# Kernel optimization log

Measured on AMD Instinct MI355X. Metric: run time of the kernel, lower is better.

The kernel has to match this reference:

```python
import jax, jax.numpy as jnp
import numpy as np

B, S, D, H, NL, FE = 2, 1024, 1024, 16, 6, 4
HD = D // H
DFF = D * FE
EPS = 1e-5


def setup_inputs() -> dict:
    key = jax.random.key(0)
    ks = jax.random.split(key, 12)
    sd = 0.02
    n = lambda k, sh: (jax.random.normal(k, sh, jnp.float32) * sd)
    return {
        "x": jax.random.normal(ks[0], (B, S, D), jnp.float32),
        "pos": n(ks[1], (1, S, D)),
        "Wq": n(ks[2], (NL, HD, HD)), "bq": jnp.zeros((NL, HD), jnp.float32),
        "Wk": n(ks[3], (NL, HD, HD)), "bk": jnp.zeros((NL, HD), jnp.float32),
        "Wv": n(ks[4], (NL, HD, HD)), "bv": jnp.zeros((NL, HD), jnp.float32),
        "Wfc": n(ks[5], (NL, D, D)), "bfc": jnp.zeros((NL, D), jnp.float32),
        "ln1_w": jnp.ones((NL, D), jnp.float32), "ln1_b": jnp.zeros((NL, D), jnp.float32),
        "ln2_w": jnp.ones((NL, D), jnp.float32), "ln2_b": jnp.zeros((NL, D), jnp.float32),
        "W1": n(ks[6], (NL, D, DFF)), "b1": jnp.zeros((NL, DFF), jnp.float32),
        "W2": n(ks[7], (NL, DFF, D)), "b2": jnp.zeros((NL, D), jnp.float32),
        "lnf_w": jnp.ones((D,), jnp.float32), "lnf_b": jnp.zeros((D,), jnp.float32),
    }


def _ln(z, w, b):
    m = jnp.mean(z, axis=-1, keepdims=True)
    v = jnp.mean(jnp.square(z - m), axis=-1, keepdims=True)
    return (z - m) * jax.lax.rsqrt(v + EPS) * w + b


def reference(x, pos, Wq, bq, Wk, bk, Wv, bv, Wfc, bfc,
              ln1_w, ln1_b, ln2_w, ln2_b, W1, b1, W2, b2, lnf_w, lnf_b):
    Bx, Sx, Dx = x.shape
    causal = jnp.tril(jnp.ones((Sx, Sx), bool))  # [S,S], broadcast over b,h
    y = x + pos[:, :Sx, :]
    scale = 1.0 / jnp.sqrt(jnp.float32(HD))
    for i in range(NL):
        yh = y.reshape(Bx, Sx, H, HD)
        # per-head Linear with weights SHARED across heads (as in source)
        q = yh @ Wq[i] + bq[i]
        k = yh @ Wk[i] + bk[i]
        v = yh @ Wv[i] + bv[i]
        score = jnp.einsum("bqhd,bkhd->bhqk", q, k)
        # masked_fill(-1e20) BEFORE scaling, as in source
        score = jnp.where(causal, score, jnp.float32(-1e20)) * scale
        attn = jax.nn.softmax(score, axis=-1)
        o = jnp.einsum("bhqk,bkhd->bqhd", attn, v).reshape(Bx, Sx, D)
        o = o @ Wfc[i] + bfc[i]
        add = _ln(o + y, ln1_w[i], ln1_b[i])
        ff = jax.nn.gelu(add @ W1[i] + b1[i], approximate=False) @ W2[i] + b2[i]
        y = _ln(ff + add, ln2_w[i], ln2_b[i])
    return _ln(y, lnf_w, lnf_b)
```

## Files before the change

kernel.cpp:

```cpp
#include <hip/hip_runtime.h>
#include <hip/hip_bf16.h>
#include <math.h>

#define B_   2
#define S_   1024
#define D_   1024
#define H_   16
#define HD_  64
#define NL_  6
#define DFF_ 4096

typedef __bf16 bf16_t;
typedef bf16_t bf16x8 __attribute__((ext_vector_type(8)));
typedef bf16_t bf16x4 __attribute__((ext_vector_type(4)));
typedef float  f32x4  __attribute__((ext_vector_type(4)));

__device__ __forceinline__ float gelu_exact(float x) {
    return 0.5f * x * (1.0f + erff(x * 0.70710678118654752f));
}

__device__ __forceinline__ void gload16(const bf16_t* g, bf16_t* l) {
    __builtin_amdgcn_global_load_lds(
        (const __attribute__((address_space(1))) void*)g,
        (__attribute__((address_space(3))) void*)l, 16, 0, 0);
}

__global__ __launch_bounds__(256) void add_pos_kernel(
    const float* __restrict__ x, const float* __restrict__ pos,
    float* __restrict__ y, bf16_t* __restrict__ yb)
{
    int idx = blockIdx.x * 256 + threadIdx.x;
    f32x4 xv = *(const f32x4*)&x[idx * 4];
    f32x4 pv = *(const f32x4*)&pos[(idx & 262143) * 4];
    f32x4 o = xv + pv;
    *(f32x4*)&y[idx * 4] = o;
    *(bf16x4*)&yb[idx * 4] = __builtin_convertvector(o, bf16x4);
}

__global__ __launch_bounds__(256) void qkv_mfma_kernel(
    const bf16_t* __restrict__ yb,
    const float* __restrict__ Wq, const float* __restrict__ bq,
    const float* __restrict__ Wk, const float* __restrict__ bk,
    const float* __restrict__ Wv, const float* __restrict__ bv,
    bf16_t* __restrict__ q, bf16_t* __restrict__ k, bf16_t* __restrict__ v)
{
    __shared__ __align__(16) bf16_t As[128][72];
    __shared__ __align__(16) bf16_t Wt[3][64][72];

    int tid = threadIdx.x;
    long m0 = (long)blockIdx.x * 128;

#pragma unroll
    for (int it = 0; it < 4; ++it) {
        int c = it * 256 + tid;
        int row = c >> 3, col = (c & 7) * 8;
        *(bf16x8*)&As[row][col] = *(const bf16x8*)&yb[(m0 + row) * 64 + col];
    }
#pragma unroll
    for (int it = 0; it < 16; ++it) {
        int i = it * 256 + tid;
        int r = i >> 6, c = i & 63;
        Wt[0][c][r] = (bf16_t)Wq[i];
        Wt[1][c][r] = (bf16_t)Wk[i];
        Wt[2][c][r] = (bf16_t)Wv[i];
    }
    __syncthreads();

    int wave = tid >> 6, lane = tid & 63;
    int quad = lane >> 4, l16 = lane & 15;
    int wm = wave * 32;

    bf16x8 a[2][2];
#pragma unroll
    for (int i = 0; i < 2; ++i)
#pragma unroll
        for (int ks = 0; ks < 2; ++ks)
            a[i][ks] = *(bf16x8*)&As[wm + i * 16 + l16][ks * 32 + quad * 8];

    f32x4 acc[3][2][4];
#pragma unroll
    for (int o = 0; o < 3; ++o)
#pragma unroll
        for (int i = 0; i < 2; ++i)
#pragma unroll
            for (int j = 0; j < 4; ++j) acc[o][i][j] = (f32x4)0.f;

#pragma unroll
    for (int o = 0; o < 3; ++o)
#pragma unroll
        for (int j = 0; j < 4; ++j) {
            bf16x8 b0 = *(bf16x8*)&Wt[o][j * 16 + l16][quad * 8];
            bf16x8 b1 = *(bf16x8*)&Wt[o][j * 16 + l16][32 + quad * 8];
#pragma unroll
            for (int i = 0; i < 2; ++i) {
                acc[o][i][j] = __builtin_amdgcn_mfma_f32_16x16x32_bf16(a[i][0], b0, acc[o][i][j], 0, 0, 0);
                acc[o][i][j] = __builtin_amdgcn_mfma_f32_16x16x32_bf16(a[i][1], b1, acc[o][i][j], 0, 0, 0);
            }
        }

    bf16_t* outs[3] = { q, k, v };
    const float* biases[3] = { bq, bk, bv };
#pragma unroll
    for (int o = 0; o < 3; ++o)
#pragma unroll
        for (int j = 0; j < 4; ++j) {
            int col = j * 16 + l16;
            float bias = biases[o][col];
#pragma unroll
            for (int i = 0; i < 2; ++i) {
                long rbase = m0 + wm + i * 16 + quad * 4;
#pragma unroll
                for (int r = 0; r < 4; ++r)
                    outs[o][(rbase + r) * 64 + col] = (bf16_t)(acc[o][i][j][r] + bias);
            }
        }
}

__global__ __launch_bounds__(256) void vtrans_kernel(
    const bf16_t* __restrict__ vb, bf16_t* __restrict__ vT)
{
    __shared__ __align__(16) bf16_t L[32][72];
    int tid = threadIdx.x;
    int s0 = blockIdx.x * 32;
    int bh = blockIdx.y;
    int b = bh >> 4, h = bh & 15;
    int sr = tid >> 3, dc = (tid & 7) * 8;
    *(bf16x8*)&L[sr][dc] =
        *(const bf16x8*)&vb[(((long)b * S_ + s0 + sr) * H_ + h) * HD_ + dc];
    __syncthreads();
    int dr = tid >> 2, sg = (tid & 3) * 8;
    bf16x8 o;
#pragma unroll
    for (int j = 0; j < 8; ++j) o[j] = L[sg + j][dr];
    *(bf16x8*)&vT[((long)bh * HD_ + dr) * S_ + s0 + sg] = o;
}

__global__ __launch_bounds__(256) void attn_mfma_kernel(
    const bf16_t* __restrict__ Q, const bf16_t* __restrict__ K,
    const bf16_t* __restrict__ VT, bf16_t* __restrict__ Ob)
{
    __shared__ __align__(16) bf16_t Ks[32][72];
    __shared__ __align__(16) bf16_t Vt[64][40];
    __shared__ __align__(16) bf16_t Ps[4][16][40];

    int tid = threadIdx.x;
    int wave = tid >> 6, lane = tid & 63;
    int quad = lane >> 4, l16 = lane & 15;
    int q0 = blockIdx.x * 64;
    int bh = blockIdx.y;
    int b = bh >> 4, h = bh & 15;
    int qw = q0 + wave * 16;
    const float scale = 0.125f;
    const float MASKED = -1.25e19f;

    const bf16_t* Qbase = Q + (((long)b * S_ + qw + l16) * H_ + h) * HD_;
    bf16x8 aq0 = *(const bf16x8*)&Qbase[quad * 8];
    bf16x8 aq1 = *(const bf16x8*)&Qbase[32 + quad * 8];

    float mrun = -3.0e38f, lrun = 0.f;
    f32x4 oacc[4];
#pragma unroll
    for (int n = 0; n < 4; ++n) oacc[n] = (f32x4)0.f;

    int srow = tid >> 3, scol = (tid & 7) * 8;
    int vdr = tid >> 2, vkg = (tid & 3) * 8;
    const bf16_t* VTbase = VT + ((long)bh * HD_ + vdr) * S_ + vkg;
    int qg = qw + l16;

    int nkt = (q0 + 64) / 32;
    for (int kt = 0; kt < nkt; ++kt) {
        int k0 = kt * 32;
        __syncthreads();
        *(bf16x8*)&Ks[srow][scol] =
            *(const bf16x8*)&K[(((long)b * S_ + k0 + srow) * H_ + h) * HD_ + scol];
        *(bf16x8*)&Vt[vdr][vkg] = *(const bf16x8*)&VTbase[k0];
        __syncthreads();

        if (k0 > qw + 15) continue;

        f32x4 sc[2];
        sc[0] = (f32x4)0.f; sc[1] = (f32x4)0.f;
#pragma unroll
        for (int n = 0; n < 2; ++n) {
            bf16x8 ak0 = *(bf16x8*)&Ks[n * 16 + l16][quad * 8];
            bf16x8 ak1 = *(bf16x8*)&Ks[n * 16 + l16][32 + quad * 8];
            sc[n] = __builtin_amdgcn_mfma_f32_16x16x32_bf16(ak0, aq0, sc[n], 0, 0, 0);
            sc[n] = __builtin_amdgcn_mfma_f32_16x16x32_bf16(ak1, aq1, sc[n], 0, 0, 0);
        }
        float pmax = MASKED;
#pragma unroll
        for (int n = 0; n < 2; ++n)
#pragma unroll
            for (int r = 0; r < 4; ++r) {
                int kv = k0 + n * 16 + quad * 4 + r;
                float sv = (kv <= qg) ? sc[n][r] * scale : MASKED;
                sc[n][r] = sv;
                pmax = fmaxf(pmax, sv);
            }
        pmax = fmaxf(pmax, __shfl_xor(pmax, 16));
        pmax = fmaxf(pmax, __shfl_xor(pmax, 32));
        float mnew = fmaxf(mrun, pmax);
        float ls = 0.f;
#pragma unroll
        for (int n = 0; n < 2; ++n)
#pragma unroll
            for (int r = 0; r < 4; ++r) {
                float pv = __expf(sc[n][r] - mnew);
                sc[n][r] = pv;
                ls += pv;
            }
        ls += __shfl_xor(ls, 16);
        ls += __shfl_xor(ls, 32);
        float alpha = __expf(mrun - mnew);
        lrun = lrun * alpha + ls;
        mrun = mnew;

        *(bf16x4*)&Ps[wave][l16][quad * 4]      = __builtin_convertvector(sc[0], bf16x4);
        *(bf16x4*)&Ps[wave][l16][16 + quad * 4] = __builtin_convertvector(sc[1], bf16x4);

        f32x4 av;
#pragma unroll
        for (int r = 0; r < 4; ++r) av[r] = __shfl(alpha, quad * 4 + r);

        bf16x8 pa = *(bf16x8*)&Ps[wave][l16][quad * 8];
#pragma unroll
        for (int n = 0; n < 4; ++n) {
            bf16x8 bv = *(bf16x8*)&Vt[n * 16 + l16][quad * 8];
            oacc[n] = __builtin_amdgcn_mfma_f32_16x16x32_bf16(pa, bv, oacc[n] * av, 0, 0, 0);
        }
    }

    float inv = 1.0f / lrun;
    f32x4 iv;
#pragma unroll
    for (int r = 0; r < 4; ++r) iv[r] = __shfl(inv, quad * 4 + r);
#pragma unroll
    for (int r = 0; r < 4; ++r) {
        long rowbase = (((long)b * S_ + qw + quad * 4 + r) * H_ + h) * HD_;
#pragma unroll
        for (int n = 0; n < 4; ++n)
            Ob[rowbase + n * 16 + l16] = (bf16_t)(oacc[n][r] * iv[r]);
    }
}

__global__ void tconv_kernel(const float* __restrict__ W, bf16_t* __restrict__ Wt,
                             int Kd, int Nd)
{
    __shared__ float t[32][33];
    int tx = threadIdx.x, ty = threadIdx.y;
    int bx = blockIdx.x, by = blockIdx.y;
#pragma unroll
    for (int i = 0; i < 4; ++i)
        t[ty + i * 8][tx] = W[(size_t)(by * 32 + ty + i * 8) * Nd + bx * 32 + tx];
    __syncthreads();
#pragma unroll
    for (int i = 0; i < 4; ++i)
        Wt[(size_t)(bx * 32 + ty + i * 8) * Kd + by * 32 + tx] = (bf16_t)t[tx][ty + i * 8];
}

__global__ __launch_bounds__(256) void gemm_bt_kernel(
    const bf16_t* __restrict__ A, const bf16_t* __restrict__ Bt,
    const float* __restrict__ bias, float* __restrict__ Cf,
    bf16_t* __restrict__ Cb, int M, int N, int K, int act, size_t pstride)
{
    __shared__ __align__(16) bf16_t As[3][128 * 32];
    __shared__ __align__(16) bf16_t Bs[3][64 * 32];
    int tid = threadIdx.x;
    int wave = tid >> 6, lane = tid & 63;
    int quad = lane >> 4, l16 = lane & 15;
    int m0 = blockIdx.x * 128;
    int n0 = blockIdx.y * 64;
    int Kc = K / gridDim.z;
    int kbeg = blockIdx.z * Kc;
    float* Cfp = Cf ? Cf + (size_t)blockIdx.z * pstride : nullptr;

    int wm = (wave >> 1) * 64, wn = (wave & 1) * 32;

    int srow = lane >> 2;
    int sslot = (lane & 3) ^ (srow & 3);
    int rslot = (quad ^ (l16 & 3)) * 8;

    f32x4 acc[4][2];
#pragma unroll
    for (int i = 0; i < 4; ++i)
#pragma unroll
        for (int j = 0; j < 2; ++j) acc[i][j] = (f32x4)0.f;

    const bf16_t* Ab = A + (size_t)(m0 + srow) * K + sslot * 8;
    const bf16_t* Bb = Bt + (size_t)(n0 + wave * 16 + srow) * K + sslot * 8;
    int seg0 = wave * 2;
    int nt = Kc >> 5;

    #define STAGE(t, buf) do {                                                      \
        int kk_ = kbeg + (t) * 32;                                                  \
        gload16(Ab + (size_t)seg0 * 16 * K + kk_, &As[(buf)][seg0 * 512]);          \
        gload16(Ab + (size_t)(seg0 + 1) * 16 * K + kk_, &As[(buf)][(seg0+1) * 512]);\
        gload16(Bb + kk_, &Bs[(buf)][wave * 512]);                                  \
    } while (0)

    #define COMPUTE(buf) do {                                                       \
        bf16x8 af[4], bfr[2];                                                       \
        _Pragma("unroll")                                                           \
        for (int i = 0; i < 4; ++i)                                                 \
            af[i] = *(bf16x8*)&As[(buf)][(wm + i * 16 + l16) * 32 + rslot];         \
        _Pragma("unroll")                                                           \
        for (int j = 0; j < 2; ++j)                                                 \
            bfr[j] = *(bf16x8*)&Bs[(buf)][(wn + j * 16 + l16) * 32 + rslot];        \
        _Pragma("unroll")                                                           \
        for (int i = 0; i < 4; ++i)                                                 \
            _Pragma("unroll")                                                       \
            for (int j = 0; j < 2; ++j)                                             \
                acc[i][j] = __builtin_amdgcn_mfma_f32_16x16x32_bf16(                \
                    af[i], bfr[j], acc[i][j], 0, 0, 0);                             \
    } while (0)

    STAGE(0, 0);
    STAGE(1, 1);

    int cur = 0, pf = 2;
    for (int t = 0; t < nt - 1; ++t) {
        asm volatile("s_waitcnt vmcnt(3)" ::: "memory");
        __builtin_amdgcn_s_barrier();
        __builtin_amdgcn_sched_barrier(0);
        if (t + 2 < nt) STAGE(t + 2, pf);
        COMPUTE(cur);
        cur = (cur == 2) ? 0 : cur + 1;
        pf  = (pf  == 2) ? 0 : pf  + 1;
    }
    asm volatile("s_waitcnt vmcnt(0)" ::: "memory");
    __builtin_amdgcn_s_barrier();
    __builtin_amdgcn_sched_barrier(0);
    COMPUTE(cur);

    #undef STAGE
    #undef COMPUTE

#pragma unroll
    for (int j = 0; j < 2; ++j) {
        int col = n0 + wn + j * 16 + l16;
        float bv = (bias && blockIdx.z == 0) ? bias[col] : 0.f;
#pragma unroll
        for (int i = 0; i < 4; ++i) {
            int rbase = m0 + wm + i * 16 + quad * 4;
#pragma unroll
            for (int r = 0; r < 4; ++r) {
                float vv = acc[i][j][r] + bv;
                if (act == 1) vv = gelu_exact(vv);
                if (Cfp) Cfp[(size_t)(rbase + r) * N + col] = vv;
                if (Cb) Cb[(size_t)(rbase + r) * N + col] = (bf16_t)vv;
            }
        }
    }
}

__global__ __launch_bounds__(256) void ln_fused_kernel(
    const float* __restrict__ a0, const float* __restrict__ a1,
    const float* __restrict__ b,
    const float* __restrict__ w, const float* __restrict__ beta,
    float* __restrict__ out, bf16_t* __restrict__ outb)
{
    long row = blockIdx.x;
    int tid = threadIdx.x;
    f32x4 z = *(const f32x4*)&a0[row * D_ + tid * 4];
    if (a1) z += *(const f32x4*)&a1[row * D_ + tid * 4];
    if (b)  z += *(const f32x4*)&b[row * D_ + tid * 4];
    float s  = z[0] + z[1] + z[2] + z[3];
    float ss = z[0]*z[0] + z[1]*z[1] + z[2]*z[2] + z[3]*z[3];
#pragma unroll
    for (int off = 32; off >= 1; off >>= 1) {
        s  += __shfl_down(s, off);
        ss += __shfl_down(ss, off);
    }
    __shared__ float red[8];
    int lane = tid & 63, wid = tid >> 6;
    if (lane == 0) { red[wid * 2] = s; red[wid * 2 + 1] = ss; }
    __syncthreads();
    s  = red[0] + red[2] + red[4] + red[6];
    ss = red[1] + red[3] + red[5] + red[7];
    float mean = s * (1.0f / D_);
    float var  = ss * (1.0f / D_) - mean * mean;
    float rs = rsqrtf(var + 1e-5f);
    f32x4 wv = *(const f32x4*)&w[tid * 4];
    f32x4 bv = *(const f32x4*)&beta[tid * 4];
    f32x4 o = (z - mean) * rs * wv + bv;
    *(f32x4*)&out[row * D_ + tid * 4] = o;
    if (outb) *(bf16x4*)&outb[row * D_ + tid * 4] = __builtin_convertvector(o, bf16x4);
}

extern "C" void kernel_launch(void* const* d_in, const int* in_sizes, int n_in,
                              void* d_out, int out_size, void* d_ws, size_t ws_size,
                              hipStream_t stream)
{
    (void)in_sizes; (void)n_in; (void)out_size; (void)ws_size;
    const float* x    = (const float*)d_in[0];
    const float* pos  = (const float*)d_in[1];
    const float* Wq   = (const float*)d_in[2];
    const float* bq   = (const float*)d_in[3];
    const float* Wk   = (const float*)d_in[4];
    const float* bk   = (const float*)d_in[5];
    const float* Wv   = (const float*)d_in[6];
    const float* bv   = (const float*)d_in[7];
    const float* Wfc  = (const float*)d_in[8];
    const float* bfc  = (const float*)d_in[9];
    const float* ln1w = (const float*)d_in[10];
    const float* ln1b = (const float*)d_in[11];
    const float* ln2w = (const float*)d_in[12];
    const float* ln2b = (const float*)d_in[13];
    const float* W1   = (const float*)d_in[14];
    const float* b1   = (const float*)d_in[15];
    const float* W2   = (const float*)d_in[16];
    const float* b2   = (const float*)d_in[17];
    const float* lnfw = (const float*)d_in[18];
    const float* lnfb = (const float*)d_in[19];

    const size_t MB = 1 << 20;
    char* ws = (char*)d_ws;
    float*  y    = (float*)(ws);
    bf16_t* yb   = (bf16_t*)(ws + 8 * MB);
    bf16_t* qb   = (bf16_t*)(ws + 12 * MB);
    bf16_t* kb   = (bf16_t*)(ws + 16 * MB);
    bf16_t* vb   = (bf16_t*)(ws + 20 * MB);
    bf16_t* ob   = (bf16_t*)(ws + 24 * MB);
    float*  t1a  = (float*)(ws + 12 * MB);
    float*  t1b  = (float*)(ws + 28 * MB);
    float*  t2a  = (float*)(ws + 12 * MB);
    float*  t2b  = (float*)(ws + 20 * MB);
    float*  add  = (float*)(ws + 28 * MB);
    bf16_t* addb = (bf16_t*)(ws + 36 * MB);
    bf16_t* vTb  = (bf16_t*)(ws + 40 * MB);
    bf16_t* ffb  = (bf16_t*)(ws + 40 * MB);
    bf16_t* WT   = (bf16_t*)(ws + 56 * MB);

    const size_t pstride_wfc  = (size_t)16 * MB / sizeof(float);
    const size_t pstride_ffn2 = (size_t)8 * MB / sizeof(float);

    add_pos_kernel<<<2048, 256, 0, stream>>>(x, pos, y, yb);

    for (int i = 0; i < NL_; ++i) {
        qkv_mfma_kernel<<<256, 256, 0, stream>>>(
            yb, Wq + i * 4096, bq + i * 64, Wk + i * 4096, bk + i * 64,
            Wv + i * 4096, bv + i * 64, qb, kb, vb);

        vtrans_kernel<<<dim3(32, 32), 256, 0, stream>>>(vb, vTb);

        attn_mfma_kernel<<<dim3(16, 32), 256, 0, stream>>>(qb, kb, vTb, ob);

        tconv_kernel<<<dim3(32, 32), dim3(32, 8), 0, stream>>>(
            Wfc + (size_t)i * D_ * D_, WT, D_, D_);
        gemm_bt_kernel<<<dim3(16, 16, 2), 256, 0, stream>>>(
            ob, WT, bfc + i * D_, t1a, nullptr, 2048, D_, D_, 0, pstride_wfc);

        ln_fused_kernel<<<2048, 256, 0, stream>>>(
            t1a, t1b, y, ln1w + i * D_, ln1b + i * D_, add, addb);

        tconv_kernel<<<dim3(128, 32), dim3(32, 8), 0, stream>>>(
            W1 + (size_t)i * D_ * DFF_, WT, D_, DFF_);
        gemm_bt_kernel<<<dim3(16, 64, 1), 256, 0, stream>>>(
            addb, WT, b1 + i * DFF_, nullptr, ffb, 2048, DFF_, D_, 1, 0);

        tconv_kernel<<<dim3(32, 128), dim3(32, 8), 0, stream>>>(
            W2 + (size_t)i * DFF_ * D_, WT, DFF_, D_);
        gemm_bt_kernel<<<dim3(16, 16, 2), 256, 0, stream>>>(
            ffb, WT, b2 + i * D_, t2a, nullptr, 2048, D_, DFF_, 0, pstride_ffn2);

        ln_fused_kernel<<<2048, 256, 0, stream>>>(
            t2a, t2b, add, ln2w + i * D_, ln2b + i * D_, y, yb);
    }

    ln_fused_kernel<<<2048, 256, 0, stream>>>(
        y, nullptr, nullptr, lnfw, lnfb, (float*)d_out, nullptr);
}
```

Measured before the change: 1.242 ms.

## Load attention K/V directly into registers with double buffering; pre-convert QKV weights

The attention kernel no longer stages K and V^T tiles through shared memory behind block-wide barriers. Each wave loads its MFMA operands straight from global memory into registers, double-buffered so the next tile's loads overlap the current tile's compute. Each wave also loops only over the causal key tiles it needs instead of the block-wide count. Separately, the QKV weight transpose and bf16 conversion move into a small per-layer kernel, and the QKV GEMM reads operands directly from global memory. This trades shared-memory reuse and barriers for more global/L2 traffic and register pressure, plus an extra kernel launch per layer.

```diff
diff --git a/kernel.cpp b/kernel.cpp
--- a/kernel.cpp
+++ b/kernel.cpp
@@ -37,35 +37,30 @@
     *(bf16x4*)&yb[idx * 4] = __builtin_convertvector(o, bf16x4);
 }
 
-__global__ __launch_bounds__(256) void qkv_mfma_kernel(
-    const bf16_t* __restrict__ yb,
-    const float* __restrict__ Wq, const float* __restrict__ bq,
-    const float* __restrict__ Wk, const float* __restrict__ bk,
-    const float* __restrict__ Wv, const float* __restrict__ bv,
-    bf16_t* __restrict__ q, bf16_t* __restrict__ k, bf16_t* __restrict__ v)
-{
-    __shared__ __align__(16) bf16_t As[128][72];
-    __shared__ __align__(16) bf16_t Wt[3][64][72];
-
-    int tid = threadIdx.x;
-    long m0 = (long)blockIdx.x * 128;
-
-#pragma unroll
-    for (int it = 0; it < 4; ++it) {
-        int c = it * 256 + tid;
-        int row = c >> 3, col = (c & 7) * 8;
-        *(bf16x8*)&As[row][col] = *(const bf16x8*)&yb[(m0 + row) * 64 + col];
-    }
+__global__ __launch_bounds__(256) void wconv3_kernel(
+    const float* __restrict__ Wq, const float* __restrict__ Wk,
+    const float* __restrict__ Wv, bf16_t* __restrict__ Wt3)
+{
+    const float* srcs[3] = { Wq, Wk, Wv };
+    const float* W = srcs[blockIdx.x];
+    bf16_t* dst = Wt3 + blockIdx.x * 4096;
+    int tid = threadIdx.x;
 #pragma unroll
     for (int it = 0; it < 16; ++it) {
         int i = it * 256 + tid;
         int r = i >> 6, c = i & 63;
-        Wt[0][c][r] = (bf16_t)Wq[i];
-        Wt[1][c][r] = (bf16_t)Wk[i];
-        Wt[2][c][r] = (bf16_t)Wv[i];
-    }
-    __syncthreads();
-
+        dst[c * 64 + r] = (bf16_t)W[i];
+    }
+}
+
+__global__ __launch_bounds__(256) void qkv_mfma_kernel(
+    const bf16_t* __restrict__ yb, const bf16_t* __restrict__ Wt3,
+    const float* __restrict__ bq, const float* __restrict__ bk,
+    const float* __restrict__ bv,
+    bf16_t* __restrict__ q, bf16_t* __restrict__ k, bf16_t* __restrict__ v)
+{
+    int tid = threadIdx.x;
+    long m0 = (long)blockIdx.x * 128;
     int wave = tid >> 6, lane = tid & 63;
     int quad = lane >> 4, l16 = lane & 15;
     int wm = wave * 32;
@@ -75,7 +70,7 @@
     for (int i = 0; i < 2; ++i)
 #pragma unroll
         for (int ks = 0; ks < 2; ++ks)
-            a[i][ks] = *(bf16x8*)&As[wm + i * 16 + l16][ks * 32 + quad * 8];
+            a[i][ks] = *(const bf16x8*)&yb[(m0 + wm + i * 16 + l16) * 64 + ks * 32 + quad * 8];
 
     f32x4 acc[3][2][4];
 #pragma unroll
@@ -89,8 +84,9 @@
     for (int o = 0; o < 3; ++o)
 #pragma unroll
         for (int j = 0; j < 4; ++j) {
-            bf16x8 b0 = *(bf16x8*)&Wt[o][j * 16 + l16][quad * 8];
-            bf16x8 b1 = *(bf16x8*)&Wt[o][j * 16 + l16][32 + quad * 8];
+            const bf16_t* wb = Wt3 + o * 4096 + (j * 16 + l16) * 64;
+            bf16x8 b0 = *(const bf16x8*)&wb[quad * 8];
+            bf16x8 b1 = *(const bf16x8*)&wb[32 + quad * 8];
 #pragma unroll
             for (int i = 0; i < 2; ++i) {
                 acc[o][i][j] = __builtin_amdgcn_mfma_f32_16x16x32_bf16(a[i][0], b0, acc[o][i][j], 0, 0, 0);
@@ -139,8 +135,6 @@
     const bf16_t* __restrict__ Q, const bf16_t* __restrict__ K,
     const bf16_t* __restrict__ VT, bf16_t* __restrict__ Ob)
 {
-    __shared__ __align__(16) bf16_t Ks[32][72];
-    __shared__ __align__(16) bf16_t Vt[64][40];
     __shared__ __align__(16) bf16_t Ps[4][16][40];
 
     int tid = threadIdx.x;
@@ -162,73 +156,82 @@
 #pragma unroll
     for (int n = 0; n < 4; ++n) oacc[n] = (f32x4)0.f;
 
-    int srow = tid >> 3, scol = (tid & 7) * 8;
-    int vdr = tid >> 2, vkg = (tid & 3) * 8;
-    const bf16_t* VTbase = VT + ((long)bh * HD_ + vdr) * S_ + vkg;
+    const bf16_t* Kr = K + (((long)b * S_ + l16) * H_ + h) * HD_;
+    const bf16_t* Vr = VT + ((long)bh * HD_ + l16) * S_;
     int qg = qw + l16;
-
-    int nkt = (q0 + 64) / 32;
-    for (int kt = 0; kt < nkt; ++kt) {
-        int k0 = kt * 32;
-        __syncthreads();
-        *(bf16x8*)&Ks[srow][scol] =
-            *(const bf16x8*)&K[(((long)b * S_ + k0 + srow) * H_ + h) * HD_ + scol];
-        *(bf16x8*)&Vt[vdr][vkg] = *(const bf16x8*)&VTbase[k0];
-        __syncthreads();
-
-        if (k0 > qw + 15) continue;
-
-        f32x4 sc[2];
-        sc[0] = (f32x4)0.f; sc[1] = (f32x4)0.f;
-#pragma unroll
-        for (int n = 0; n < 2; ++n) {
-            bf16x8 ak0 = *(bf16x8*)&Ks[n * 16 + l16][quad * 8];
-            bf16x8 ak1 = *(bf16x8*)&Ks[n * 16 + l16][32 + quad * 8];
-            sc[n] = __builtin_amdgcn_mfma_f32_16x16x32_bf16(ak0, aq0, sc[n], 0, 0, 0);
-            sc[n] = __builtin_amdgcn_mfma_f32_16x16x32_bf16(ak1, aq1, sc[n], 0, 0, 0);
-        }
-        float pmax = MASKED;
-#pragma unroll
-        for (int n = 0; n < 2; ++n)
-#pragma unroll
-            for (int r = 0; r < 4; ++r) {
-                int kv = k0 + n * 16 + quad * 4 + r;
-                float sv = (kv <= qg) ? sc[n][r] * scale : MASKED;
-                sc[n][r] = sv;
-                pmax = fmaxf(pmax, sv);
-            }
-        pmax = fmaxf(pmax, __shfl_xor(pmax, 16));
-        pmax = fmaxf(pmax, __shfl_xor(pmax, 32));
-        float mnew = fmaxf(mrun, pmax);
-        float ls = 0.f;
-#pragma unroll
-        for (int n = 0; n < 2; ++n)
-#pragma unroll
-            for (int r = 0; r < 4; ++r) {
-                float pv = __expf(sc[n][r] - mnew);
-                sc[n][r] = pv;
-                ls += pv;
-            }
-        ls += __shfl_xor(ls, 16);
-        ls += __shfl_xor(ls, 32);
-        float alpha = __expf(mrun - mnew);
-        lrun = lrun * alpha + ls;
-        mrun = mnew;
-
-        *(bf16x4*)&Ps[wave][l16][quad * 4]      = __builtin_convertvector(sc[0], bf16x4);
-        *(bf16x4*)&Ps[wave][l16][16 + quad * 4] = __builtin_convertvector(sc[1], bf16x4);
-
-        f32x4 av;
-#pragma unroll
-        for (int r = 0; r < 4; ++r) av[r] = __shfl(alpha, quad * 4 + r);
-
-        bf16x8 pa = *(bf16x8*)&Ps[wave][l16][quad * 8];
-#pragma unroll
-        for (int n = 0; n < 4; ++n) {
-            bf16x8 bv = *(bf16x8*)&Vt[n * 16 + l16][quad * 8];
-            oacc[n] = __builtin_amdgcn_mfma_f32_16x16x32_bf16(pa, bv, oacc[n] * av, 0, 0, 0);
-        }
-    }
+    int nkt = (qw + 47) >> 5;
+
+    #define LOADKV(k0_, ak_, pv_) do {                                          \
+        _Pragma("unroll")                                                       \
+        for (int n = 0; n < 2; ++n) {                                           \
+            const bf16_t* kr_ = Kr + (long)((k0_) + n * 16) * (H_ * HD_);       \
+            ak_[n][0] = *(const bf16x8*)&kr_[quad * 8];                         \
+            ak_[n][1] = *(const bf16x8*)&kr_[32 + quad * 8];                    \
+        }                                                                       \
+        _Pragma("unroll")                                                       \
+        for (int n = 0; n < 4; ++n)                                             \
+            pv_[n] = *(const bf16x8*)&Vr[(long)n * 16 * S_ + (k0_) + quad * 8]; \
+    } while (0)
+
+    #define TILE(k0_, ak_, pv_) do {                                            \
+        f32x4 sc[2];                                                            \
+        sc[0] = (f32x4)0.f; sc[1] = (f32x4)0.f;                                 \
+        _Pragma("unroll")                                                       \
+        for (int n = 0; n < 2; ++n) {                                           \
+            sc[n] = __builtin_amdgcn_mfma_f32_16x16x32_bf16(ak_[n][0], aq0, sc[n], 0, 0, 0); \
+            sc[n] = __builtin_amdgcn_mfma_f32_16x16x32_bf16(ak_[n][1], aq1, sc[n], 0, 0, 0); \
+        }                                                                       \
+        float pmax = MASKED;                                                    \
+        _Pragma("unroll")                                                       \
+        for (int n = 0; n < 2; ++n)                                             \
+            _Pragma("unroll")                                                   \
+            for (int r = 0; r < 4; ++r) {                                       \
+                int kv = (k0_) + n * 16 + quad * 4 + r;                         \
+                float sv = (kv <= qg) ? sc[n][r] * scale : MASKED;              \
+                sc[n][r] = sv;                                                  \
+                pmax = fmaxf(pmax, sv);                                         \
+            }                                                                   \
+        pmax = fmaxf(pmax, __shfl_xor(pmax, 16));                               \
+        pmax = fmaxf(pmax, __shfl_xor(pmax, 32));                               \
+        float mnew = fmaxf(mrun, pmax);                                         \
+        float ls = 0.f;                                                         \
+        _Pragma("unroll")                                                       \
+        for (int n = 0; n < 2; ++n)                                             \
+            _Pragma("unroll")                                                   \
+            for (int r = 0; r < 4; ++r) {                                       \
+                float pval = __expf(sc[n][r] - mnew);                           \
+                sc[n][r] = pval;                                                \
+                ls += pval;                                                     \
+            }                                                                   \
+        ls += __shfl_xor(ls, 16);                                               \
+        ls += __shfl_xor(ls, 32);                                               \
+        float alpha = __expf(mrun - mnew);                                      \
+        lrun = lrun * alpha + ls;                                               \
+        mrun = mnew;                                                            \
+        *(bf16x4*)&Ps[wave][l16][quad * 4]      = __builtin_convertvector(sc[0], bf16x4); \
+        *(bf16x4*)&Ps[wave][l16][16 + quad * 4] = __builtin_convertvector(sc[1], bf16x4); \
+        f32x4 av;                                                               \
+        _Pragma("unroll")                                                       \
+        for (int r = 0; r < 4; ++r) av[r] = __shfl(alpha, quad * 4 + r);        \
+        bf16x8 pa = *(bf16x8*)&Ps[wave][l16][quad * 8];                         \
+        _Pragma("unroll")                                                       \
+        for (int n = 0; n < 4; ++n)                                             \
+            oacc[n] = __builtin_amdgcn_mfma_f32_16x16x32_bf16(pa, pv_[n], oacc[n] * av, 0, 0, 0); \
+    } while (0)
+
+    bf16x8 akA[2][2], pvA[4], akB[2][2], pvB[4];
+    LOADKV(0, akA, pvA);
+    int kt = 0;
+    while (true) {
+        if (kt + 1 < nkt) LOADKV((kt + 1) * 32, akB, pvB);
+        TILE(kt * 32, akA, pvA);
+        ++kt; if (kt >= nkt) break;
+        if (kt + 1 < nkt) LOADKV((kt + 1) * 32, akA, pvA);
+        TILE(kt * 32, akB, pvB);
+        ++kt; if (kt >= nkt) break;
+    }
+    #undef LOADKV
+    #undef TILE
 
     float inv = 1.0f / lrun;
     f32x4 iv;
@@ -430,6 +433,7 @@
     bf16_t* vTb  = (bf16_t*)(ws + 40 * MB);
     bf16_t* ffb  = (bf16_t*)(ws + 40 * MB);
     bf16_t* WT   = (bf16_t*)(ws + 56 * MB);
+    bf16_t* WT3  = (bf16_t*)(ws + 56 * MB);
 
     const size_t pstride_wfc  = (size_t)16 * MB / sizeof(float);
     const size_t pstride_ffn2 = (size_t)8 * MB / sizeof(float);
@@ -437,9 +441,10 @@
     add_pos_kernel<<<2048, 256, 0, stream>>>(x, pos, y, yb);
 
     for (int i = 0; i < NL_; ++i) {
+        wconv3_kernel<<<3, 256, 0, stream>>>(
+            Wq + i * 4096, Wk + i * 4096, Wv + i * 4096, WT3);
         qkv_mfma_kernel<<<256, 256, 0, stream>>>(
-            yb, Wq + i * 4096, bq + i * 64, Wk + i * 4096, bk + i * 64,
-            Wv + i * 4096, bv + i * 64, qb, kb, vb);
+            yb, WT3, bq + i * 64, bk + i * 64, bv + i * 64, qb, kb, vb);
 
         vtrans_kernel<<<dim3(32, 32), 256, 0, stream>>>(vb, vTb);
 
```

After: 1.399 ms. +12.6%, slower.
